# Performance work log

Measured on AMD Instinct MI355X. Metric: run time of the kernel, lower is better.

## Reference

```python
import jax, jax.numpy as jnp
import numpy as np


def setup_inputs() -> dict:
    key = jax.random.key(0)
    k1, k2 = jax.random.split(key)
    B, H, W, D = 4096, 64, 64, 512
    inputs = jax.random.normal(k1, (B, D), dtype=jnp.float32)
    # keras 'random_uniform' initializer default range [-0.05, 0.05]
    weights_map = jax.random.uniform(k2, (H, W, D), dtype=jnp.float32,
                                     minval=-0.05, maxval=0.05)
    return {"inputs": inputs, "weights_map": weights_map}


def reference(inputs, weights_map):
    # inputs: (B, D); weights_map: (H, W, D)
    H, W, D = weights_map.shape
    flat_w = weights_map.reshape(-1, D)              # (N, D), N = H*W
    # avoids materializing the (B, N, D) difference tensor)
    x_sq = jnp.sum(inputs * inputs, axis=1, keepdims=True)    # (B, 1)
    w_sq = jnp.sum(flat_w * flat_w, axis=1)                   # (N,)
    sq_dist = x_sq - 2.0 * (inputs @ flat_w.T) + w_sq         # (B, N)
    sq_dist = jnp.maximum(sq_dist, 0.0)
    bmu_flat = jnp.argmin(sq_dist, axis=1)                    # (B,)
    bmu_y = (bmu_flat // W).astype(jnp.int32)
    bmu_x = (bmu_flat % W).astype(jnp.int32)
    bmu_indices = jnp.stack([bmu_y, bmu_x], axis=1)           # (B, 2)
    min_sq = jnp.take_along_axis(sq_dist, bmu_flat[:, None], axis=1)[:, 0]
    quantization_errors = jnp.sqrt(min_sq)                    # (B,)
    return bmu_indices, quantization_errors
```

## Files before the change

kernel.cpp:

```cpp
#include <hip/hip_runtime.h>

#define B_ROWS 4096
#define N_COLS 4096
#define DIM    512
#define LDK    1024

typedef __attribute__((ext_vector_type(8))) short short8;
typedef __attribute__((ext_vector_type(4))) float floatx4;

__device__ __forceinline__ unsigned short f2bf_rn(float f) {
    unsigned u = __float_as_uint(f);
    u += 0x7fffu + ((u >> 16) & 1u);
    return (unsigned short)(u >> 16);
}
__device__ __forceinline__ float bf2f(unsigned short h) {
    return __uint_as_float(((unsigned)h) << 16);
}

__device__ __forceinline__ unsigned long long pack_key(float v, int idx) {
    unsigned u = __float_as_uint(v);
    u = (u & 0x80000000u) ? ~u : (u | 0x80000000u);
    return ((unsigned long long)u << 32) | (unsigned)idx;
}

__device__ __forceinline__ void async16(const unsigned short* g, unsigned short* l) {
    __builtin_amdgcn_global_load_lds(
        (__attribute__((address_space(1))) void*)g,
        (__attribute__((address_space(3))) void*)l, 16, 0, 0);
}

__global__ __launch_bounds__(256) void som_convert(
    const float* __restrict__ X, const float* __restrict__ Wt,
    unsigned short* __restrict__ Xc, unsigned short* __restrict__ Wc,
    float* __restrict__ x_sq, float* __restrict__ w_sq,
    unsigned long long* __restrict__ packed)
{
    int wave = threadIdx.x >> 6, lane = threadIdx.x & 63;
    int grow = blockIdx.x * 4 + wave;
    bool isX = grow < B_ROWS;
    const float* src = isX ? (X + (size_t)grow * DIM)
                           : (Wt + (size_t)(grow - B_ROWS) * DIM);
    const float4* p4 = (const float4*)src;
    float4 a = p4[lane * 2], b = p4[lane * 2 + 1];
    float f[8] = {a.x, a.y, a.z, a.w, b.x, b.y, b.z, b.w};
    unsigned short hi[8], lo[8];
    float s = 0.f;
    #pragma unroll
    for (int t = 0; t < 8; ++t) {
        hi[t] = f2bf_rn(f[t]);
        lo[t] = f2bf_rn(f[t] - bf2f(hi[t]));
        s = fmaf(f[t], f[t], s);
    }
    unsigned short* dst = (isX ? Xc + (size_t)grow * LDK
                               : Wc + (size_t)(grow - B_ROWS) * LDK) + lane * 8;
    *(ushort4*)(dst)       = make_ushort4(hi[0], hi[1], hi[2], hi[3]);
    *(ushort4*)(dst + 4)   = make_ushort4(hi[4], hi[5], hi[6], hi[7]);
    *(ushort4*)(dst + 512) = make_ushort4(lo[0], lo[1], lo[2], lo[3]);
    *(ushort4*)(dst + 516) = make_ushort4(lo[4], lo[5], lo[6], lo[7]);
    #pragma unroll
    for (int off = 32; off >= 1; off >>= 1) s += __shfl_xor(s, off, 64);
    if (lane == 0) {
        if (isX) { x_sq[grow] = s; packed[grow] = ~0ull; }
        else     { w_sq[grow - B_ROWS] = s; }
    }
}

__global__ __launch_bounds__(256, 3) void som_dist_bf16(
    const unsigned short* __restrict__ Xc, const unsigned short* __restrict__ Wc,
    const float* __restrict__ w_sq, unsigned long long* __restrict__ packed)
{
    __shared__ unsigned short Ah[128 * 32];
    __shared__ unsigned short Al[128 * 32];
    __shared__ unsigned short Bh[128 * 32];
    __shared__ unsigned short Bl[128 * 32];
    const int tid  = threadIdx.x;
    const int wave = tid >> 6, lane = tid & 63;
    const int wr = wave >> 1, wc = wave & 1;
    const int bm = blockIdx.y, bn = blockIdx.x;
    const int quad = lane >> 4, t16 = lane & 15;

    const int srow = lane >> 2;
    const int scol = (lane & 3) * 8;
    const unsigned short* gAh = Xc + (size_t)(bm * 128 + wave * 32 + srow) * LDK + scol;
    const unsigned short* gBh = Wc + (size_t)(bn * 128 + wave * 32 + srow) * LDK + scol;
    const unsigned short* gAl = gAh + 512;
    const unsigned short* gBl = gBh + 512;
    unsigned short* lAh = &Ah[(wave * 32) * 32];
    unsigned short* lAl = &Al[(wave * 32) * 32];
    unsigned short* lBh = &Bh[(wave * 32) * 32];
    unsigned short* lBl = &Bl[(wave * 32) * 32];

    const unsigned short* pah = &Ah[(wr * 64 + t16) * 32 + quad * 8];
    const unsigned short* pal = &Al[(wr * 64 + t16) * 32 + quad * 8];
    const unsigned short* pbh = &Bh[(wc * 64 + t16) * 32 + quad * 8];
    const unsigned short* pbl = &Bl[(wc * 64 + t16) * 32 + quad * 8];

    floatx4 acc[4][4];
    #pragma unroll
    for (int i = 0; i < 4; ++i)
        #pragma unroll
        for (int j = 0; j < 4; ++j) acc[i][j] = (floatx4){0.f, 0.f, 0.f, 0.f};

    #pragma unroll 1
    for (int k0 = 0; k0 < DIM; k0 += 32) {
        __syncthreads();
        async16(gAh + k0,            lAh);
        async16(gAh + k0 + 16 * LDK, lAh + 16 * 32);
        async16(gAl + k0,            lAl);
        async16(gAl + k0 + 16 * LDK, lAl + 16 * 32);
        async16(gBh + k0,            lBh);
        async16(gBh + k0 + 16 * LDK, lBh + 16 * 32);
        async16(gBl + k0,            lBl);
        async16(gBl + k0 + 16 * LDK, lBl + 16 * 32);
        __syncthreads();

        short8 ah[4], bh[4], x[4];
        #pragma unroll
        for (int i = 0; i < 4; ++i) ah[i] = *(const short8*)(pah + i * 16 * 32);
        #pragma unroll
        for (int j = 0; j < 4; ++j) bh[j] = *(const short8*)(pbh + j * 16 * 32);
        #pragma unroll
        for (int i = 0; i < 4; ++i)
            #pragma unroll
            for (int j = 0; j < 4; ++j)
                acc[i][j] = __builtin_amdgcn_mfma_f32_16x16x32_bf16(
                    ah[i], bh[j], acc[i][j], 0, 0, 0);

        #pragma unroll
        for (int j = 0; j < 4; ++j) x[j] = *(const short8*)(pbl + j * 16 * 32);
        #pragma unroll
        for (int i = 0; i < 4; ++i)
            #pragma unroll
            for (int j = 0; j < 4; ++j)
                acc[i][j] = __builtin_amdgcn_mfma_f32_16x16x32_bf16(
                    ah[i], x[j], acc[i][j], 0, 0, 0);

        #pragma unroll
        for (int i = 0; i < 4; ++i) x[i] = *(const short8*)(pal + i * 16 * 32);
        #pragma unroll
        for (int i = 0; i < 4; ++i)
            #pragma unroll
            for (int j = 0; j < 4; ++j)
                acc[i][j] = __builtin_amdgcn_mfma_f32_16x16x32_bf16(
                    x[i], bh[j], acc[i][j], 0, 0, 0);
    }

    const int col0 = bn * 128 + wc * 64 + t16;
    float wq[4];
    #pragma unroll
    for (int j = 0; j < 4; ++j) wq[j] = w_sq[col0 + j * 16];
    const int row_base = bm * 128 + wr * 64 + quad * 4;
    #pragma unroll
    for (int i = 0; i < 4; ++i) {
        #pragma unroll
        for (int r = 0; r < 4; ++r) {
            unsigned long long best = ~0ull;
            #pragma unroll
            for (int j = 0; j < 4; ++j) {
                float val = fmaf(-2.f, acc[i][j][r], wq[j]);
                unsigned long long key = pack_key(val, col0 + j * 16);
                best = (key < best) ? key : best;
            }
            #pragma unroll
            for (int m = 1; m <= 8; m <<= 1) {
                unsigned long long o = __shfl_xor(best, m, 64);
                best = (o < best) ? o : best;
            }
            if (t16 == 0)
                atomicMin(&packed[row_base + i * 16 + r], best);
        }
    }
}

__global__ __launch_bounds__(256) void som_finalize(
    const unsigned long long* __restrict__ packed,
    const float* __restrict__ x_sq, float* __restrict__ out)
{
    int b = blockIdx.x * 256 + threadIdx.x;
    unsigned long long p = packed[b];
    unsigned idx = (unsigned)(p & 0xffffffffull);
    unsigned key = (unsigned)(p >> 32);
    unsigned u = (key & 0x80000000u) ? (key & 0x7fffffffu) : ~key;
    float val = __uint_as_float(u);
    float sq = fmaxf(x_sq[b] + val, 0.f);
    out[2 * b]     = (float)(idx >> 6);
    out[2 * b + 1] = (float)(idx & 63);
    out[2 * B_ROWS + b] = sqrtf(sq);
}

extern "C" void kernel_launch(void* const* d_in, const int* in_sizes, int n_in,
                              void* d_out, int out_size, void* d_ws, size_t ws_size,
                              hipStream_t stream) {
    const float* X  = (const float*)d_in[0];
    const float* Wt = (const float*)d_in[1];
    float* out = (float*)d_out;

    unsigned long long* packed = (unsigned long long*)d_ws;
    float* x_sq = (float*)((char*)d_ws + (32 << 10));
    float* w_sq = (float*)((char*)d_ws + (48 << 10));
    unsigned short* Xc = (unsigned short*)((char*)d_ws + (64 << 10));
    unsigned short* Wc = (unsigned short*)((char*)d_ws + (64 << 10) + ((size_t)B_ROWS * LDK * 2));

    som_convert<<<dim3((B_ROWS + N_COLS) / 4), dim3(256), 0, stream>>>(
        X, Wt, Xc, Wc, x_sq, w_sq, packed);
    som_dist_bf16<<<dim3(N_COLS / 128, B_ROWS / 128), dim3(256), 0, stream>>>(
        Xc, Wc, w_sq, packed);
    som_finalize<<<dim3(B_ROWS / 256), dim3(256), 0, stream>>>(packed, x_sq, out);
}
```

Before: 123.4 us.

## Fuse convert, distance GEMM and finalize into one persistent kernel with grid barriers

Merges the three launches into a single kernel of 1024 blocks. Each block converts eight rows to split bf16 and computes their norms, then waits at a global atomic barrier before running its 128x128 distance tile and atomic argmin. The first 16 blocks wait on a second counter and then write the final outputs. This removes two kernel launch gaps in exchange for spin-wait barriers and an added memset. It relies on all 1024 blocks being co-resident (4 per CU under the launch bound), otherwise it deadlocks.

Result: slower. 248.2 us (+101.1%).

```diff
diff --git a/kernel.cpp b/kernel.cpp
--- a/kernel.cpp
+++ b/kernel.cpp
@@ -4,6 +4,8 @@
 #define N_COLS 4096
 #define DIM    512
 #define LDK    1024
+#define GRID   1024
+#define FINAL_BLOCKS 16
 
 typedef __attribute__((ext_vector_type(8))) short short8;
 typedef __attribute__((ext_vector_type(4))) float floatx4;
@@ -29,45 +31,13 @@
         (__attribute__((address_space(3))) void*)l, 16, 0, 0);
 }
 
-__global__ __launch_bounds__(256) void som_convert(
+__global__ __launch_bounds__(256, 4) void som_fused(
     const float* __restrict__ X, const float* __restrict__ Wt,
     unsigned short* __restrict__ Xc, unsigned short* __restrict__ Wc,
     float* __restrict__ x_sq, float* __restrict__ w_sq,
-    unsigned long long* __restrict__ packed)
-{
-    int wave = threadIdx.x >> 6, lane = threadIdx.x & 63;
-    int grow = blockIdx.x * 4 + wave;
-    bool isX = grow < B_ROWS;
-    const float* src = isX ? (X + (size_t)grow * DIM)
-                           : (Wt + (size_t)(grow - B_ROWS) * DIM);
-    const float4* p4 = (const float4*)src;
-    float4 a = p4[lane * 2], b = p4[lane * 2 + 1];
-    float f[8] = {a.x, a.y, a.z, a.w, b.x, b.y, b.z, b.w};
-    unsigned short hi[8], lo[8];
-    float s = 0.f;
-    #pragma unroll
-    for (int t = 0; t < 8; ++t) {
-        hi[t] = f2bf_rn(f[t]);
-        lo[t] = f2bf_rn(f[t] - bf2f(hi[t]));
-        s = fmaf(f[t], f[t], s);
-    }
-    unsigned short* dst = (isX ? Xc + (size_t)grow * LDK
-                               : Wc + (size_t)(grow - B_ROWS) * LDK) + lane * 8;
-    *(ushort4*)(dst)       = make_ushort4(hi[0], hi[1], hi[2], hi[3]);
-    *(ushort4*)(dst + 4)   = make_ushort4(hi[4], hi[5], hi[6], hi[7]);
-    *(ushort4*)(dst + 512) = make_ushort4(lo[0], lo[1], lo[2], lo[3]);
-    *(ushort4*)(dst + 516) = make_ushort4(lo[4], lo[5], lo[6], lo[7]);
-    #pragma unroll
-    for (int off = 32; off >= 1; off >>= 1) s += __shfl_xor(s, off, 64);
-    if (lane == 0) {
-        if (isX) { x_sq[grow] = s; packed[grow] = ~0ull; }
-        else     { w_sq[grow - B_ROWS] = s; }
-    }
-}
-
-__global__ __launch_bounds__(256, 3) void som_dist_bf16(
-    const unsigned short* __restrict__ Xc, const unsigned short* __restrict__ Wc,
-    const float* __restrict__ w_sq, unsigned long long* __restrict__ packed)
+    unsigned long long* __restrict__ packed,
+    unsigned* __restrict__ sync0, unsigned* __restrict__ sync1,
+    float* __restrict__ out)
 {
     __shared__ unsigned short Ah[128 * 32];
     __shared__ unsigned short Al[128 * 32];
@@ -75,8 +45,50 @@
     __shared__ unsigned short Bl[128 * 32];
     const int tid  = threadIdx.x;
     const int wave = tid >> 6, lane = tid & 63;
+
+    #pragma unroll
+    for (int rr = 0; rr < 2; ++rr) {
+        int grow = blockIdx.x * 8 + rr * 4 + wave;
+        bool isX = grow < B_ROWS;
+        const float* src = isX ? (X + (size_t)grow * DIM)
+                               : (Wt + (size_t)(grow - B_ROWS) * DIM);
+        const float4* p4 = (const float4*)src;
+        float4 a = p4[lane * 2], b = p4[lane * 2 + 1];
+        float f[8] = {a.x, a.y, a.z, a.w, b.x, b.y, b.z, b.w};
+        unsigned short hi[8], lo[8];
+        float s = 0.f;
+        #pragma unroll
+        for (int t = 0; t < 8; ++t) {
+            hi[t] = f2bf_rn(f[t]);
+            lo[t] = f2bf_rn(f[t] - bf2f(hi[t]));
+            s = fmaf(f[t], f[t], s);
+        }
+        unsigned short* dst = (isX ? Xc + (size_t)grow * LDK
+                                   : Wc + (size_t)(grow - B_ROWS) * LDK) + lane * 8;
+        *(ushort4*)(dst)       = make_ushort4(hi[0], hi[1], hi[2], hi[3]);
+        *(ushort4*)(dst + 4)   = make_ushort4(hi[4], hi[5], hi[6], hi[7]);
+        *(ushort4*)(dst + 512) = make_ushort4(lo[0], lo[1], lo[2], lo[3]);
+        *(ushort4*)(dst + 516) = make_ushort4(lo[4], lo[5], lo[6], lo[7]);
+        #pragma unroll
+        for (int off = 32; off >= 1; off >>= 1) s += __shfl_xor(s, off, 64);
+        if (lane == 0) {
+            if (isX) { x_sq[grow] = s; packed[grow] = ~0ull; }
+            else     { w_sq[grow - B_ROWS] = s; }
+        }
+    }
+
+    __syncthreads();
+    if (tid == 0) {
+        __threadfence();
+        __hip_atomic_fetch_add(sync0, 1u, __ATOMIC_ACQ_REL, __HIP_MEMORY_SCOPE_AGENT);
+        while (__hip_atomic_load(sync0, __ATOMIC_ACQUIRE, __HIP_MEMORY_SCOPE_AGENT) < GRID)
+            __builtin_amdgcn_s_sleep(2);
+        __threadfence();
+    }
+    __syncthreads();
+
+    const int bm = blockIdx.x >> 5, bn = blockIdx.x & 31;
     const int wr = wave >> 1, wc = wave & 1;
-    const int bm = blockIdx.y, bn = blockIdx.x;
     const int quad = lane >> 4, t16 = lane & 15;
 
     const int srow = lane >> 2;
@@ -145,47 +157,61 @@
                     x[i], bh[j], acc[i][j], 0, 0, 0);
     }
 
-    const int col0 = bn * 128 + wc * 64 + t16;
-    float wq[4];
-    #pragma unroll
-    for (int j = 0; j < 4; ++j) wq[j] = w_sq[col0 + j * 16];
-    const int row_base = bm * 128 + wr * 64 + quad * 4;
-    #pragma unroll
-    for (int i = 0; i < 4; ++i) {
-        #pragma unroll
-        for (int r = 0; r < 4; ++r) {
-            unsigned long long best = ~0ull;
-            #pragma unroll
-            for (int j = 0; j < 4; ++j) {
-                float val = fmaf(-2.f, acc[i][j][r], wq[j]);
-                unsigned long long key = pack_key(val, col0 + j * 16);
-                best = (key < best) ? key : best;
+    {
+        const int col0 = bn * 128 + wc * 64 + t16;
+        float wq[4];
+        #pragma unroll
+        for (int j = 0; j < 4; ++j) wq[j] = w_sq[col0 + j * 16];
+        const int row_base = bm * 128 + wr * 64 + quad * 4;
+        #pragma unroll
+        for (int i = 0; i < 4; ++i) {
+            #pragma unroll
+            for (int r = 0; r < 4; ++r) {
+                unsigned long long best = ~0ull;
+                #pragma unroll
+                for (int j = 0; j < 4; ++j) {
+                    float val = fmaf(-2.f, acc[i][j][r], wq[j]);
+                    unsigned long long key = pack_key(val, col0 + j * 16);
+                    best = (key < best) ? key : best;
+                }
+                #pragma unroll
+                for (int m = 1; m <= 8; m <<= 1) {
+                    unsigned long long o = __shfl_xor(best, m, 64);
+                    best = (o < best) ? o : best;
+                }
+                if (t16 == 0)
+                    atomicMin(&packed[row_base + i * 16 + r], best);
             }
-            #pragma unroll
-            for (int m = 1; m <= 8; m <<= 1) {
-                unsigned long long o = __shfl_xor(best, m, 64);
-                best = (o < best) ? o : best;
-            }
-            if (t16 == 0)
-                atomicMin(&packed[row_base + i * 16 + r], best);
         }
     }
-}
-
-__global__ __launch_bounds__(256) void som_finalize(
-    const unsigned long long* __restrict__ packed,
-    const float* __restrict__ x_sq, float* __restrict__ out)
-{
-    int b = blockIdx.x * 256 + threadIdx.x;
-    unsigned long long p = packed[b];
-    unsigned idx = (unsigned)(p & 0xffffffffull);
-    unsigned key = (unsigned)(p >> 32);
-    unsigned u = (key & 0x80000000u) ? (key & 0x7fffffffu) : ~key;
-    float val = __uint_as_float(u);
-    float sq = fmaxf(x_sq[b] + val, 0.f);
-    out[2 * b]     = (float)(idx >> 6);
-    out[2 * b + 1] = (float)(idx & 63);
-    out[2 * B_ROWS + b] = sqrtf(sq);
+
+    __syncthreads();
+    if (tid == 0) {
+        __threadfence();
+        __hip_atomic_fetch_add(sync1, 1u, __ATOMIC_ACQ_REL, __HIP_MEMORY_SCOPE_AGENT);
+    }
+    if (blockIdx.x >= FINAL_BLOCKS) return;
+
+    if (tid == 0) {
+        while (__hip_atomic_load(sync1, __ATOMIC_ACQUIRE, __HIP_MEMORY_SCOPE_AGENT) < GRID)
+            __builtin_amdgcn_s_sleep(2);
+        __threadfence();
+    }
+    __syncthreads();
+
+    {
+        int b = blockIdx.x * 256 + tid;
+        unsigned long long p = __hip_atomic_load(&packed[b], __ATOMIC_RELAXED,
+                                                 __HIP_MEMORY_SCOPE_AGENT);
+        unsigned idx = (unsigned)(p & 0xffffffffull);
+        unsigned key = (unsigned)(p >> 32);
+        unsigned u = (key & 0x80000000u) ? (key & 0x7fffffffu) : ~key;
+        float val = __uint_as_float(u);
+        float sq = fmaxf(x_sq[b] + val, 0.f);
+        out[2 * b]     = (float)(idx >> 6);
+        out[2 * b + 1] = (float)(idx & 63);
+        out[2 * B_ROWS + b] = sqrtf(sq);
+    }
 }
 
 extern "C" void kernel_launch(void* const* d_in, const int* in_sizes, int n_in,
@@ -198,12 +224,11 @@
     unsigned long long* packed = (unsigned long long*)d_ws;
     float* x_sq = (float*)((char*)d_ws + (32 << 10));
     float* w_sq = (float*)((char*)d_ws + (48 << 10));
-    unsigned short* Xc = (unsigned short*)((char*)d_ws + (64 << 10));
-    unsigned short* Wc = (unsigned short*)((char*)d_ws + (64 << 10) + ((size_t)B_ROWS * LDK * 2));
-
-    som_convert<<<dim3((B_ROWS + N_COLS) / 4), dim3(256), 0, stream>>>(
-        X, Wt, Xc, Wc, x_sq, w_sq, packed);
-    som_dist_bf16<<<dim3(N_COLS / 128, B_ROWS / 128), dim3(256), 0, stream>>>(
-        Xc, Wc, w_sq, packed);
-    som_finalize<<<dim3(B_ROWS / 256), dim3(256), 0, stream>>>(packed, x_sq, out);
-}
+    unsigned* syncb = (unsigned*)((char*)d_ws + (64 << 10));
+    unsigned short* Xc = (unsigned short*)((char*)d_ws + (72 << 10));
+    unsigned short* Wc = (unsigned short*)((char*)d_ws + (72 << 10) + ((size_t)B_ROWS * LDK * 2));
+
+    hipMemsetAsync(syncb, 0, 256, stream);
+    som_fused<<<dim3(GRID), dim3(256), 0, stream>>>(
+        X, Wt, Xc, Wc, x_sq, w_sq, packed, syncb, syncb + 1, out);
+}
```
